# Kernel tuning notes

Hardware: AMD Instinct MI355X
Metric: run time of the kernel (lower is better)

## Reference

```python
import jax, jax.numpy as jnp
import numpy as np

D_MODEL = 192
D_INNER = 384   # expand=2
D_STATE = 16
D_CONV = 4
DT_RANK = 12    # ceil(192/16)
DEPTH = 4
STRIDE = 4
N_PATCH = 400   # 1600 // 4
NCLS = 1000
BATCH = 32
EPS = 1e-5


def setup_inputs() -> dict:
    key = jax.random.key(0)
    ks = iter(jax.random.split(key, 64))
    nrm = lambda shp, s=0.02: jax.random.normal(next(ks), shp, jnp.float32) * s
    inp = {}
    inp["imgs"] = jax.random.normal(next(ks), (BATCH, 1, 40, 40), jnp.float32)
    # StrideEmbed: conv1d(kernel=stride=4) == per-patch linear on [B,400,4]
    inp["patch_w"] = nrm((STRIDE, D_MODEL))
    inp["patch_b"] = jnp.zeros((D_MODEL,), jnp.float32)
    inp["cls_token"] = nrm((1, 1, D_MODEL))
    inp["pos_embed"] = nrm((1, N_PATCH + 1, D_MODEL))
    # per-block Mamba params, stacked on a leading depth axis
    inp["norm_ws"] = jnp.ones((DEPTH, D_MODEL), jnp.float32)
    inp["in_proj_ws"] = nrm((DEPTH, D_MODEL, 2 * D_INNER))
    inp["conv_ws"] = nrm((DEPTH, D_INNER, D_CONV), 0.2)
    inp["conv_bs"] = jnp.zeros((DEPTH, D_INNER), jnp.float32)
    inp["x_proj_ws"] = nrm((DEPTH, D_INNER, DT_RANK + 2 * D_STATE))
    inp["dt_proj_ws"] = nrm((DEPTH, DT_RANK, D_INNER), 0.1)
    # dt bias ~ inverse-softplus of small positive dt
    inp["dt_proj_bs"] = jnp.log(jnp.expm1(jnp.full((DEPTH, D_INNER), 0.01, jnp.float32)))
    inp["A_logs"] = jnp.log(jnp.broadcast_to(
        jnp.arange(1, D_STATE + 1, dtype=jnp.float32), (DEPTH, D_INNER, D_STATE)))
    inp["Ds"] = jnp.ones((DEPTH, D_INNER), jnp.float32)
    inp["out_proj_ws"] = nrm((DEPTH, D_INNER, D_MODEL))
    inp["norm_f_w"] = jnp.ones((D_MODEL,), jnp.float32)
    inp["head_w"] = nrm((D_MODEL, NCLS))
    inp["head_b"] = jnp.zeros((NCLS,), jnp.float32)
    return inp


def rmsnorm(x, w):
    return x * jax.lax.rsqrt(jnp.mean(x * x, axis=-1, keepdims=True) + EPS) * w


def mamba_mixer(x, in_w, conv_w, conv_b, xp_w, dt_w, dt_b, A_log, Dp, out_w):
    # x: [B, L, D_MODEL]
    B, L, _ = x.shape
    xz = x @ in_w                         # [B, L, 2*d_inner]
    u, z = jnp.split(xz, 2, axis=-1)
    # causal depthwise conv1d (kernel 4), truncated to L, then SiLU
    upad = jnp.pad(u, ((0, 0), (D_CONV - 1, 0), (0, 0)))
    uc = sum(upad[:, k:k + L, :] * conv_w[:, k] for k in range(D_CONV)) + conv_b
    uc = jax.nn.silu(uc)
    # input-dependent dt, B, C
    dbl = uc @ xp_w                       # [B, L, dt_rank + 2*d_state]
    dt = dbl[..., :DT_RANK]
    Bm = dbl[..., DT_RANK:DT_RANK + D_STATE]
    Cm = dbl[..., DT_RANK + D_STATE:]
    delta = jax.nn.softplus(dt @ dt_w + dt_b)           # [B, L, d_inner]
    A = -jnp.exp(A_log)                                  # [d_inner, d_state]
    dA = jnp.exp(delta[..., None] * A)                   # [B, L, d_inner, d_state]
    dBu = (delta * uc)[..., None] * Bm[:, :, None, :]    # [B, L, d_inner, d_state]

    def step(h, t):
        da, dbu, c = t
        h = da * h + dbu                                 # [B, d_inner, d_state]
        y = jnp.einsum('bds,bs->bd', h, c)
        return h, y

    h0 = jnp.zeros((B, D_INNER, D_STATE), x.dtype)
    _, ys = jax.lax.scan(step, h0, (jnp.moveaxis(dA, 1, 0),
                                    jnp.moveaxis(dBu, 1, 0),
                                    jnp.moveaxis(Cm, 1, 0)))
    y = jnp.moveaxis(ys, 0, 1) + uc * Dp                 # [B, L, d_inner]
    return (y * jax.nn.silu(z)) @ out_w


def reference(imgs, patch_w, patch_b, cls_token, pos_embed, norm_ws, in_proj_ws,
              conv_ws, conv_bs, x_proj_ws, dt_proj_ws, dt_proj_bs, A_logs, Ds,
              out_proj_ws, norm_f_w, head_w, head_b):
    B = imgs.shape[0]
    seq = imgs.reshape(B, N_PATCH, STRIDE)               # [B, 400, 4] (in_chans=1)
    x = seq @ patch_w + patch_b + pos_embed[:, :-1, :]   # patch embed + pos (cls pos is last)
    cls = cls_token + pos_embed[:, -1:, :]
    x = jnp.concatenate([x, jnp.broadcast_to(cls, (B, 1, D_MODEL))], axis=1)  # cls appended at end
    residual = None
    for i in range(DEPTH):
        residual = x if residual is None else x + residual  # fused add-norm, prenorm
        h = rmsnorm(residual, norm_ws[i])
        x = mamba_mixer(h, in_proj_ws[i], conv_ws[i], conv_bs[i], x_proj_ws[i],
                        dt_proj_ws[i], dt_proj_bs[i], A_logs[i], Ds[i], out_proj_ws[i])
    x = rmsnorm(x + residual, norm_f_w)                   # final fused add-norm, prenorm=False
    return x[:, -1, :] @ head_w + head_b                  # head on cls (last) token
```

## Files before the change

### kernel.cpp

```cpp
#include <hip/hip_runtime.h>
#include <hip/hip_bf16.h>
#include <hip/hip_fp16.h>

using bf16 = __hip_bfloat16;
typedef short short8 __attribute__((ext_vector_type(8)));
typedef float floatx4 __attribute__((ext_vector_type(4)));

#define LSEQ 401
#define NTOK 12832
#define NTOKP 12928
#define DM 192
#define DI 384
#define NB 32
#define NCH 13
#define CHT 32
#define LOG2E 1.4426950408889634f

#define O_IMGS   0
#define O_PW     51200
#define O_PB     51968
#define O_CLS    52160
#define O_POS    52352
#define O_NORMW  129344
#define O_INW    130112
#define O_CONVW  719936
#define O_CONVB  726080
#define O_XPW    727616
#define O_DTW    795200
#define O_DTB    813632
#define O_ALOG   815168
#define O_DS     839744
#define O_OUTW   841280
#define O_NORMF  1136192
#define O_HEADW  1136384
#define O_HEADB  1328384
#define WTOT     1329408

#define BO_INWT  0
#define BO_XPWT  589824
#define BO_OUTWT 688128
#define BFTOT_F  491520

__constant__ int g_sz[18] = {51200, 768, 192, 192, 76992, 768, 589824, 6144, 1536,
                             67584, 18432, 1536, 24576, 1536, 294912, 192, 192000, 1000};
__constant__ int g_off[18] = {O_IMGS, O_PW, O_PB, O_CLS, O_POS, O_NORMW, O_INW, O_CONVW,
                              O_CONVB, O_XPW, O_DTW, O_DTB, O_ALOG, O_DS, O_OUTW,
                              O_NORMF, O_HEADW, O_HEADB};

struct SrcPtrs { const void* p[18]; };

static __device__ __forceinline__ int probe_flag(const unsigned short* probe) {
    unsigned short u0 = probe[0];
    if (u0 == 0x3F80u) return 0;
    if (u0 == 0x3C00u) return 2;
    return 1;
}
static __device__ __forceinline__ float load_src(int flag, const void* p, long i) {
    if (flag == 0) return __bfloat162float(((const bf16*)p)[i]);
    if (flag == 2) return __half2float(((const __half*)p)[i]);
    return ((const float*)p)[i];
}
static __device__ __forceinline__ unsigned short f2b(float f) {
    bf16 h = __float2bfloat16(f);
    return *reinterpret_cast<unsigned short*>(&h);
}
static __device__ __forceinline__ float b2f_us(unsigned short us) {
    unsigned int ui = (unsigned int)us << 16;
    return __uint_as_float(ui);
}
static __device__ __forceinline__ float exp2fast(float x) {
    return __builtin_amdgcn_exp2f(x);
}

__global__ void convert_kernel(SrcPtrs sp, const unsigned short* __restrict__ probe,
                               float* __restrict__ dst) {
    int flag = probe_flag(probe);
    int which = blockIdx.y;
    int n = g_sz[which];
    const void* src = sp.p[which];
    float* d = dst + g_off[which];
    for (int i = blockIdx.x * blockDim.x + threadIdx.x; i < n; i += gridDim.x * blockDim.x)
        d[i] = load_src(flag, src, i);
}

__global__ void prep_wt_kernel(SrcPtrs sp, const unsigned short* __restrict__ probe,
                               unsigned short* __restrict__ bfw) {
    int flag = probe_flag(probe);
    int which = blockIdx.y, layer = blockIdx.z;
    int i = blockIdx.x * 256 + threadIdx.x;
    if (which == 0) {
        if (i >= 768 * 192) return;
        int n = i / 192, k = i % 192;
        float v = load_src(flag, sp.p[6], (long)layer * 147456 + (long)k * 768 + n);
        bfw[BO_INWT + (long)layer * 147456 + i] = f2b(v);
    } else if (which == 1) {
        if (i >= 64 * 384) return;
        int n = i / 384, k = i % 384;
        float v = (n < 44) ? load_src(flag, sp.p[9], (long)layer * 16896 + (long)k * 44 + n) : 0.f;
        bfw[BO_XPWT + (long)layer * 24576 + i] = f2b(v);
    } else {
        if (i >= 192 * 384) return;
        int n = i / 384, k = i % 384;
        float v = load_src(flag, sp.p[14], (long)layer * 73728 + (long)k * 192 + n);
        bfw[BO_OUTWT + (long)layer * 73728 + i] = f2b(v);
    }
}

__global__ __launch_bounds__(256) void resnorm_kernel(
    const float* __restrict__ x, float* __restrict__ res, unsigned short* __restrict__ hbf,
    const float* __restrict__ w, const float* __restrict__ W, int first) {
    int wv = threadIdx.x >> 6, lane = threadIdx.x & 63;
    long tok = (long)blockIdx.x * 4 + wv;
    long base = tok * DM + lane * 4;
    float4 v = make_float4(0.f, 0.f, 0.f, 0.f);
    bool real = (tok < NTOK);
    if (real && lane < 48) {
        if (first) {
            int b = (int)(tok / LSEQ), t = (int)(tok % LSEQ);
            int c = lane * 4;
            if (t < 400) {
                float s0 = W[O_IMGS + b * 1600 + t * 4 + 0];
                float s1 = W[O_IMGS + b * 1600 + t * 4 + 1];
                float s2 = W[O_IMGS + b * 1600 + t * 4 + 2];
                float s3 = W[O_IMGS + b * 1600 + t * 4 + 3];
                float4 p0 = *(const float4*)(W + O_PW + 0 * DM + c);
                float4 p1 = *(const float4*)(W + O_PW + 1 * DM + c);
                float4 p2 = *(const float4*)(W + O_PW + 2 * DM + c);
                float4 p3 = *(const float4*)(W + O_PW + 3 * DM + c);
                float4 pb = *(const float4*)(W + O_PB + c);
                float4 ps = *(const float4*)(W + O_POS + t * DM + c);
                v.x = s0 * p0.x + s1 * p1.x + s2 * p2.x + s3 * p3.x + pb.x + ps.x;
                v.y = s0 * p0.y + s1 * p1.y + s2 * p2.y + s3 * p3.y + pb.y + ps.y;
                v.z = s0 * p0.z + s1 * p1.z + s2 * p2.z + s3 * p3.z + pb.z + ps.z;
                v.w = s0 * p0.w + s1 * p1.w + s2 * p2.w + s3 * p3.w + pb.w + ps.w;
            } else {
                float4 cl = *(const float4*)(W + O_CLS + c);
                float4 ps = *(const float4*)(W + O_POS + 400 * DM + c);
                v.x = cl.x + ps.x; v.y = cl.y + ps.y;
                v.z = cl.z + ps.z; v.w = cl.w + ps.w;
            }
        } else {
            v = *(const float4*)(x + base);
            float4 r = *(const float4*)(res + base);
            v.x += r.x; v.y += r.y; v.z += r.z; v.w += r.w;
        }
        *(float4*)(res + base) = v;
    }
    float ss = v.x * v.x + v.y * v.y + v.z * v.z + v.w * v.w;
#pragma unroll
    for (int o = 1; o < 64; o <<= 1) ss += __shfl_xor(ss, o, 64);
    float inv = rsqrtf(ss * (1.f / DM) + 1e-5f);
    if (lane < 48) {
        if (real) {
            float4 w4 = *(const float4*)(w + lane * 4);
            ushort4 h;
            h.x = f2b(v.x * inv * w4.x); h.y = f2b(v.y * inv * w4.y);
            h.z = f2b(v.z * inv * w4.z); h.w = f2b(v.w * inv * w4.w);
            *(ushort4*)(hbf + base) = h;
        } else if (tok < NTOKP) {
            ushort4 h; h.x = h.y = h.z = h.w = 0;
            *(ushort4*)(hbf + base) = h;
        }
    }
}

template <int OUTBF>
__global__ __launch_bounds__(256) void gemm_mfma(
    const unsigned short* __restrict__ A, const unsigned short* __restrict__ Wt,
    void* __restrict__ C, int K, int N, int NC) {
    __shared__ unsigned short sA[64][72];
    __shared__ unsigned short sW[64][72];
    int tid = threadIdx.x;
    int w = tid >> 6, lane = tid & 63;
    int q = lane >> 4, m = lane & 15;
    long tok0 = (long)blockIdx.x * 64;
    int n0 = blockIdx.y * 64;
    floatx4 acc[4] = {};
    for (int k0 = 0; k0 < K; k0 += 64) {
        int slot = tid;
#pragma unroll
        for (int i = 0; i < 2; ++i, slot += 256) {
            int r = slot >> 3, c8 = (slot & 7) * 8;
            *(short8*)&sA[r][c8] = *(const short8*)(A + (tok0 + r) * K + k0 + c8);
            *(short8*)&sW[r][c8] = *(const short8*)(Wt + (long)(n0 + r) * K + k0 + c8);
        }
        __syncthreads();
#pragma unroll
        for (int q2 = 0; q2 < 64; q2 += 32) {
            short8 bfr = *(const short8*)&sA[w * 16 + m][q2 + q * 8];
#pragma unroll
            for (int nt = 0; nt < 4; ++nt) {
                short8 afr = *(const short8*)&sW[nt * 16 + m][q2 + q * 8];
                acc[nt] = __builtin_amdgcn_mfma_f32_16x16x32_bf16(afr, bfr, acc[nt], 0, 0, 0);
            }
        }
        __syncthreads();
    }
    long tok = tok0 + w * 16 + m;
#pragma unroll
    for (int nt = 0; nt < 4; ++nt) {
        int ch = n0 + nt * 16 + q * 4;
        if (OUTBF) {
            unsigned short* dst = (unsigned short*)C + tok * NC + ch;
            ushort4 h4;
            h4.x = f2b(acc[nt][0]); h4.y = f2b(acc[nt][1]);
            h4.z = f2b(acc[nt][2]); h4.w = f2b(acc[nt][3]);
            *(ushort4*)dst = h4;
        } else {
            float* dst = (float*)C + tok * NC + ch;
            if (ch + 3 < N) {
                *(float4*)dst = make_float4(acc[nt][0], acc[nt][1], acc[nt][2], acc[nt][3]);
            } else {
#pragma unroll
                for (int r = 0; r < 4; ++r)
                    if (ch + r < N) dst[r] = acc[nt][r];
            }
        }
    }
}

__global__ __launch_bounds__(256) void gemm_mfma128(
    const unsigned short* __restrict__ A, const unsigned short* __restrict__ Wt,
    unsigned short* __restrict__ C, int K, int NC) {
    __shared__ unsigned short sA[128][72];
    __shared__ unsigned short sW[64][72];
    int tid = threadIdx.x;
    int w = tid >> 6, lane = tid & 63;
    int q = lane >> 4, m = lane & 15;
    long tok0 = (long)blockIdx.x * 128;
    int n0 = blockIdx.y * 64;
    floatx4 acc[2][4] = {};
    for (int k0 = 0; k0 < K; k0 += 64) {
#pragma unroll
        for (int p = 0; p < 4; ++p) {
            int idx = tid + p * 256;
            int r = idx >> 3, c8 = (idx & 7) * 8;
            *(short8*)&sA[r][c8] = *(const short8*)(A + (tok0 + r) * K + k0 + c8);
        }
#pragma unroll
        for (int p = 0; p < 2; ++p) {
            int idx = tid + p * 256;
            int r = idx >> 3, c8 = (idx & 7) * 8;
            *(short8*)&sW[r][c8] = *(const short8*)(Wt + (long)(n0 + r) * K + k0 + c8);
        }
        __syncthreads();
#pragma unroll
        for (int q2 = 0; q2 < 64; q2 += 32) {
#pragma unroll
            for (int tf = 0; tf < 2; ++tf) {
                short8 bfr = *(const short8*)&sA[w * 32 + tf * 16 + m][q2 + q * 8];
#pragma unroll
                for (int nt = 0; nt < 4; ++nt) {
                    short8 afr = *(const short8*)&sW[nt * 16 + m][q2 + q * 8];
                    acc[tf][nt] = __builtin_amdgcn_mfma_f32_16x16x32_bf16(afr, bfr, acc[tf][nt], 0, 0, 0);
                }
            }
        }
        __syncthreads();
    }
#pragma unroll
    for (int tf = 0; tf < 2; ++tf) {
        long tok = tok0 + w * 32 + tf * 16 + m;
#pragma unroll
        for (int nt = 0; nt < 4; ++nt) {
            int ch = n0 + nt * 16 + q * 4;
            ushort4 h4;
            h4.x = f2b(acc[tf][nt][0]); h4.y = f2b(acc[tf][nt][1]);
            h4.z = f2b(acc[tf][nt][2]); h4.w = f2b(acc[tf][nt][3]);
            *(ushort4*)((unsigned short*)C + tok * NC + ch) = h4;
        }
    }
}

__global__ __launch_bounds__(256) void gemm_xproj_conv(
    const unsigned short* __restrict__ xzb, const unsigned short* __restrict__ Wt,
    const float* __restrict__ cw, const float* __restrict__ cb,
    unsigned short* __restrict__ ucb, float* __restrict__ dblP) {
    __shared__ unsigned short sA[64][72];
    __shared__ unsigned short sW[64][72];
    __shared__ float scw[128][4];
    __shared__ float scb[128];
    int tid = threadIdx.x;
    int w = tid >> 6, lane = tid & 63;
    int q = lane >> 4, m = lane & 15;
    long tok0 = (long)blockIdx.x * 64;
    int koff = blockIdx.y * 128;
    float* C = dblP + (long)blockIdx.y * NTOKP * 44;
    if (tid < 128) {
        scb[tid] = cb[koff + tid];
        *(float4*)&scw[tid][0] = *(const float4*)(cw + (koff + tid) * 4);
    }
    floatx4 acc[4] = {};
    for (int k0 = 0; k0 < 128; k0 += 64) {
        if (k0 == 0) __syncthreads();
        int slot = tid;
#pragma unroll
        for (int i = 0; i < 2; ++i, slot += 256) {
            int r = slot >> 3, c8 = (slot & 7) * 8;
            long tok = tok0 + r;
            int t = (int)(tok % LSEQ);
            int lk = k0 + c8;
            int kk = koff + lk;
            float res[8];
#pragma unroll
            for (int jj = 0; jj < 8; ++jj) res[jj] = scb[lk + jj];
#pragma unroll
            for (int j = 0; j < 4; ++j) {
                int off = 3 - j;
                if (t >= off) {
                    short8 v = *(const short8*)(xzb + (tok - off) * 768 + kk);
#pragma unroll
                    for (int jj = 0; jj < 8; ++jj)
                        res[jj] = fmaf(scw[lk + jj][j], b2f_us((unsigned short)v[jj]), res[jj]);
                }
            }
            short8 h8;
#pragma unroll
            for (int jj = 0; jj < 8; ++jj) {
                float sv = res[jj] / (1.f + __expf(-res[jj]));
                h8[jj] = (short)f2b(sv);
            }
            *(short8*)&sA[r][c8] = h8;
            *(short8*)(ucb + tok * DI + kk) = h8;
            *(short8*)&sW[r][c8] = *(const short8*)(Wt + (long)r * DI + koff + k0 + c8);
        }
        __syncthreads();
#pragma unroll
        for (int q2 = 0; q2 < 64; q2 += 32) {
            short8 bfr = *(const short8*)&sA[w * 16 + m][q2 + q * 8];
#pragma unroll
            for (int nt = 0; nt < 4; ++nt) {
                short8 afr = *(const short8*)&sW[nt * 16 + m][q2 + q * 8];
                acc[nt] = __builtin_amdgcn_mfma_f32_16x16x32_bf16(afr, bfr, acc[nt], 0, 0, 0);
            }
        }
        __syncthreads();
    }
    long tok = tok0 + w * 16 + m;
#pragma unroll
    for (int nt = 0; nt < 4; ++nt) {
        int ch = nt * 16 + q * 4;
        float* dst = C + tok * 44 + ch;
        if (ch + 3 < 44) {
            *(float4*)dst = make_float4(acc[nt][0], acc[nt][1], acc[nt][2], acc[nt][3]);
        } else {
#pragma unroll
            for (int r = 0; r < 4; ++r)
                if (ch + r < 44) dst[r] = acc[nt][r];
        }
    }
}

__global__ __launch_bounds__(256) void dbl_sum_kernel(const float* __restrict__ dblP,
                                                      float* __restrict__ dbl) {
    int i = blockIdx.x * 256 + threadIdx.x;
    if (i < NTOK * 44)
        dbl[i] = dblP[i] + dblP[(long)NTOKP * 44 + i] + dblP[(long)2 * NTOKP * 44 + i];
}

__global__ __launch_bounds__(256) void scan_sum_kernel(
    const float* __restrict__ dbl, const unsigned short* __restrict__ ucb,
    const float* __restrict__ dtw, const float* __restrict__ dtb,
    const float* __restrict__ Alog, unsigned short* __restrict__ deltaBuf,
    float* __restrict__ Aprod, float* __restrict__ Hend) {
    int ch = blockIdx.x, b = blockIdx.y;
    int tid = threadIdx.x;
    int shalf = tid & 1;
    int d = blockIdx.z * 128 + (tid >> 1);
    int t0 = ch * CHT;
    long tokb = (long)b * LSEQ + t0;
    int tmax = min(CHT, LSEQ - t0);
    bool last = (ch == NCH - 1);
    __shared__ float sdt[CHT][12];
    __shared__ float sB[CHT][16];
    for (int i = tid; i < tmax * 12; i += 256) {
        int r = i / 12, k = i % 12;
        sdt[r][k] = dbl[(tokb + r) * 44 + k];
    }
    if (!last) {
        for (int i = tid; i < CHT * 16; i += 256) {
            int r = i >> 4, s = i & 15;
            sB[r][s] = dbl[(tokb + r) * 44 + 12 + s];
        }
    }
    float dtwr[12];
#pragma unroll
    for (int k = 0; k < 12; ++k) dtwr[k] = dtw[k * DI + d];
    float bias = dtb[d];
    float a[8];
#pragma unroll
    for (int s = 0; s < 8; ++s) a[s] = -__expf(Alog[d * 16 + shalf * 8 + s]) * LOG2E;
    float h[8] = {};
    float sumd = 0.f;
    __syncthreads();
    float u0 = b2f_us(ucb[tokb * DI + d]);
    float u1 = b2f_us(ucb[(tokb + min(1, tmax - 1)) * DI + d]);
#pragma unroll 2
    for (int t = 0; t < tmax; ++t) {
        int tp = min(t + 2, tmax - 1);
        float u2 = b2f_us(ucb[(tokb + tp) * DI + d]);
        float acc = bias;
#pragma unroll
        for (int k = 0; k < 12; ++k) acc = fmaf(sdt[t][k], dtwr[k], acc);
        float delta = (acc > 20.f) ? acc : __logf(1.f + __expf(acc));
        delta = b2f_us(f2b(delta));
        if (shalf == 0) deltaBuf[(tokb + t) * DI + d] = f2b(delta);
        if (!last) {
            float du = delta * u0;
            sumd += delta;
            float Bv[8];
            *(float4*)&Bv[0] = *(const float4*)&sB[t][shalf * 8];
            *(float4*)&Bv[4] = *(const float4*)&sB[t][shalf * 8 + 4];
#pragma unroll
            for (int s = 0; s < 8; ++s) {
                float da = exp2fast(delta * a[s]);
                h[s] = fmaf(da, h[s], du * Bv[s]);
            }
        }
        u0 = u1; u1 = u2;
    }
    if (!last) {
        long idx = (((long)b * NCH + ch) * DI + d) * 16 + shalf * 8;
        float ap[8], he[8];
#pragma unroll
        for (int s = 0; s < 8; ++s) { ap[s] = exp2fast(a[s] * sumd); he[s] = h[s]; }
        *(float4*)(Aprod + idx) = *(float4*)&ap[0];
        *(float4*)(Aprod + idx + 4) = *(float4*)&ap[4];
        *(float4*)(Hend + idx) = *(float4*)&he[0];
        *(float4*)(Hend + idx + 4) = *(float4*)&he[4];
    }
}

__global__ __launch_bounds__(256) void scan_combine_kernel(
    const float* __restrict__ Ap, const float* __restrict__ He, float* __restrict__ hinit) {
    long gid = (long)blockIdx.x * 256 + threadIdx.x;
    int b = (int)(gid / 6144);
    int r = (int)(gid % 6144);
    float carry = 0.f;
#pragma unroll
    for (int j = 0; j < NCH; ++j) {
        long idx = ((long)b * NCH + j) * 6144 + r;
        hinit[idx] = carry;
        if (j < NCH - 1) carry = fmaf(Ap[idx], carry, He[idx]);
    }
}

__global__ __launch_bounds__(256) void scan_main_kernel(
    const unsigned short* __restrict__ deltaBuf, const unsigned short* __restrict__ ucb,
    const unsigned short* __restrict__ xzb, const float* __restrict__ Alog,
    const float* __restrict__ Dvec, const float* __restrict__ hinit,
    const float* __restrict__ dbl, unsigned short* __restrict__ ybf) {
    int ch = blockIdx.x, b = blockIdx.y;
    int tid = threadIdx.x;
    int shalf = tid & 1;
    int d = blockIdx.z * 128 + (tid >> 1);
    int t0 = ch * CHT;
    long tokb = (long)b * LSEQ + t0;
    int tmax = min(CHT, LSEQ - t0);
    __shared__ float sB[CHT][16], sC[CHT][16];
    for (int i = tid; i < CHT * 16; i += 256) {
        int r = i >> 4, s = i & 15;
        bool ok = (r < tmax);
        sB[r][s] = ok ? dbl[(tokb + r) * 44 + 12 + s] : 0.f;
        sC[r][s] = ok ? dbl[(tokb + r) * 44 + 28 + s] : 0.f;
    }
    float a[8];
#pragma unroll
    for (int s = 0; s < 8; ++s) a[s] = -__expf(Alog[d * 16 + shalf * 8 + s]) * LOG2E;
    float h[8];
    long hidx = (((long)b * NCH + ch) * DI + d) * 16 + shalf * 8;
    *(float4*)&h[0] = *(const float4*)(hinit + hidx);
    *(float4*)&h[4] = *(const float4*)(hinit + hidx + 4);
    float Dp = Dvec[d];
    __syncthreads();
    int t1i = min(1, tmax - 1);
    float d0 = b2f_us(deltaBuf[tokb * DI + d]);
    float u0 = b2f_us(ucb[tokb * DI + d]);
    float z0 = b2f_us(xzb[tokb * 768 + DI + d]);
    float d1 = b2f_us(deltaBuf[(tokb + t1i) * DI + d]);
    float u1 = b2f_us(ucb[(tokb + t1i) * DI + d]);
    float z1 = b2f_us(xzb[(tokb + t1i) * 768 + DI + d]);
#pragma unroll 2
    for (int t = 0; t < tmax; ++t) {
        int tp = min(t + 2, tmax - 1);
        float d2 = b2f_us(deltaBuf[(tokb + tp) * DI + d]);
        float u2 = b2f_us(ucb[(tokb + tp) * DI + d]);
        float z2 = b2f_us(xzb[(tokb + tp) * 768 + DI + d]);
        float Bv[8], Cv[8];
        *(float4*)&Bv[0] = *(const float4*)&sB[t][shalf * 8];
        *(float4*)&Bv[4] = *(const float4*)&sB[t][shalf * 8 + 4];
        *(float4*)&Cv[0] = *(const float4*)&sC[t][shalf * 8];
        *(float4*)&Cv[4] = *(const float4*)&sC[t][shalf * 8 + 4];
        float du = d0 * u0;
        float y0 = 0.f, y1 = 0.f, y2 = 0.f, y3 = 0.f;
#pragma unroll
        for (int s = 0; s < 8; s += 4) {
            float da0 = exp2fast(d0 * a[s]);
            float da1 = exp2fast(d0 * a[s + 1]);
            float da2 = exp2fast(d0 * a[s + 2]);
            float da3 = exp2fast(d0 * a[s + 3]);
            h[s]     = fmaf(da0, h[s],     du * Bv[s]);
            h[s + 1] = fmaf(da1, h[s + 1], du * Bv[s + 1]);
            h[s + 2] = fmaf(da2, h[s + 2], du * Bv[s + 2]);
            h[s + 3] = fmaf(da3, h[s + 3], du * Bv[s + 3]);
            y0 = fmaf(h[s],     Cv[s],     y0);
            y1 = fmaf(h[s + 1], Cv[s + 1], y1);
            y2 = fmaf(h[s + 2], Cv[s + 2], y2);
            y3 = fmaf(h[s + 3], Cv[s + 3], y3);
        }
        float p = (y0 + y1) + (y2 + y3);
        p += __shfl_xor(p, 1, 64);
        if (shalf == 0) {
            float y = fmaf(u0, Dp, p);
            float gz = z0 / (1.f + __expf(-z0));
            ybf[(tokb + t) * DI + d] = f2b(y * gz);
        }
        d0 = d1; u0 = u1; z0 = z1;
        d1 = d2; u1 = u2; z1 = z2;
    }
}

__global__ __launch_bounds__(128) void head_kernel(
    const float* __restrict__ x, const float* __restrict__ res,
    const float* __restrict__ nf, const float* __restrict__ hw,
    const float* __restrict__ hb, const unsigned short* __restrict__ probe,
    void* __restrict__ out) {
    int b = blockIdx.y;
    int n = blockIdx.x * 128 + threadIdx.x;
    long tok = (long)b * LSEQ + 400;
    __shared__ float vs[DM];
    __shared__ float red[2];
    float ss = 0.f;
    for (int i = threadIdx.x; i < DM; i += 128) {
        float v = x[tok * DM + i] + res[tok * DM + i];
        vs[i] = v;
        ss = fmaf(v, v, ss);
    }
#pragma unroll
    for (int o = 1; o < 64; o <<= 1) ss += __shfl_xor(ss, o, 64);
    if ((threadIdx.x & 63) == 0) red[threadIdx.x >> 6] = ss;
    __syncthreads();
    float inv = rsqrtf((red[0] + red[1]) * (1.f / DM) + 1e-5f);
    for (int i = threadIdx.x; i < DM; i += 128) vs[i] = vs[i] * inv * nf[i];
    __syncthreads();
    if (n < 1000) {
        float acc = hb[n];
#pragma unroll 4
        for (int c = 0; c < DM; ++c) acc = fmaf(vs[c], hw[c * 1000 + n], acc);
        int flag = probe_flag(probe);
        if (flag == 0)      ((bf16*)out)[b * 1000 + n] = (bf16)acc;
        else if (flag == 2) ((__half*)out)[b * 1000 + n] = __float2half(acc);
        else                ((float*)out)[b * 1000 + n] = acc;
    }
}

extern "C" void kernel_launch(void* const* d_in, const int* in_sizes, int n_in,
                              void* d_out, int out_size, void* d_ws, size_t ws_size,
                              hipStream_t stream) {
    float* ws = (float*)d_ws;
    float* Wr = ws;
    unsigned short* bfw = (unsigned short*)(ws + WTOT);
    float* act   = ws + WTOT + BFTOT_F;
    float* resT  = act;
    float* xB    = resT + (long)NTOKP * DM;
    float* dbl   = xB + (long)NTOKP * DM;
    float* dblP  = dbl + (long)NTOKP * 44;
    float* Aprod = dblP + (long)3 * NTOKP * 44;
    float* Hend  = Aprod + (long)NB * NCH * 6144;
    float* hinit = Hend + (long)NB * NCH * 6144;
    unsigned short* deltaB = (unsigned short*)(hinit + (long)NB * NCH * 6144);
    unsigned short* hbf = deltaB + (long)NTOKP * DI;
    unsigned short* xzb = hbf + (long)NTOKP * DM;
    unsigned short* ucb = xzb + (long)NTOKP * 768;
    unsigned short* ybf = ucb + (long)NTOKP * DI;

    const unsigned short* probe = (const unsigned short*)d_in[5];

    SrcPtrs sp;
    for (int i = 0; i < 18; ++i) sp.p[i] = d_in[i];
    convert_kernel<<<dim3(64, 18), 256, 0, stream>>>(sp, probe, Wr);
    prep_wt_kernel<<<dim3(576, 3, 4), 256, 0, stream>>>(sp, probe, bfw);

    for (int i = 0; i < 4; ++i) {
        resnorm_kernel<<<NTOKP / 4, 256, 0, stream>>>(
            xB, resT, hbf, Wr + O_NORMW + i * DM, Wr, i == 0);
        gemm_mfma128<<<dim3(101, 12), 256, 0, stream>>>(
            hbf, bfw + BO_INWT + (long)i * 147456, xzb, 192, 768);
        gemm_xproj_conv<<<dim3(202, 3), 256, 0, stream>>>(
            xzb, bfw + BO_XPWT + (long)i * 24576,
            Wr + O_CONVW + i * 1536, Wr + O_CONVB + i * DI, ucb, dblP);
        dbl_sum_kernel<<<(NTOK * 44 + 255) / 256, 256, 0, stream>>>(dblP, dbl);
        scan_sum_kernel<<<dim3(NCH, NB, 3), 256, 0, stream>>>(
            dbl, ucb, Wr + O_DTW + i * 4608, Wr + O_DTB + i * DI,
            Wr + O_ALOG + i * 6144, deltaB, Aprod, Hend);
        scan_combine_kernel<<<(NB * 6144) / 256, 256, 0, stream>>>(Aprod, Hend, hinit);
        scan_main_kernel<<<dim3(NCH, NB, 3), 256, 0, stream>>>(
            deltaB, ucb, xzb, Wr + O_ALOG + i * 6144, Wr + O_DS + i * DI,
            hinit, dbl, ybf);
        gemm_mfma<0><<<dim3(202, 3), 256, 0, stream>>>(
            ybf, bfw + BO_OUTWT + (long)i * 73728, xB, 384, 192, 192);
    }

    head_kernel<<<dim3(8, NB), 128, 0, stream>>>(
        xB, resT, Wr + O_NORMF, Wr + O_HEADW, Wr + O_HEADB, probe, d_out);
}
```

Measured before the change: 603.7 us.

## Fuse split-K partial reduction into scan_sum and halve scan chunk length

Removes the separate dbl_sum kernel. scan_sum now sums the three split-K partial x_proj slabs directly into shared memory, and the z==0 blocks write the reduced dbl back for later kernels. It also halves the chunk length (CHT 32→16, NCH 13→26), doubling the number of scan blocks so the sequential chunked scan has more parallelism. The cost is more chunk states for scan_combine to process and redundant partial-sum reads across the three z-blocks. It also assumes scan_combine and scan_main use NCH/CHT consistently.

```diff
diff --git a/kernel.cpp b/kernel.cpp
--- a/kernel.cpp
+++ b/kernel.cpp
@@ -12,8 +12,9 @@
 #define DM 192
 #define DI 384
 #define NB 32
-#define NCH 13
-#define CHT 32
+#define NCH 26
+#define CHT 16
+#define SLAB ((long)NTOKP * 44)
 #define LOG2E 1.4426950408889634f
 
 #define O_IMGS   0
@@ -351,18 +352,11 @@
     }
 }
 
-__global__ __launch_bounds__(256) void dbl_sum_kernel(const float* __restrict__ dblP,
-                                                      float* __restrict__ dbl) {
-    int i = blockIdx.x * 256 + threadIdx.x;
-    if (i < NTOK * 44)
-        dbl[i] = dblP[i] + dblP[(long)NTOKP * 44 + i] + dblP[(long)2 * NTOKP * 44 + i];
-}
-
 __global__ __launch_bounds__(256) void scan_sum_kernel(
-    const float* __restrict__ dbl, const unsigned short* __restrict__ ucb,
+    const float* __restrict__ dblP, const unsigned short* __restrict__ ucb,
     const float* __restrict__ dtw, const float* __restrict__ dtb,
     const float* __restrict__ Alog, unsigned short* __restrict__ deltaBuf,
-    float* __restrict__ Aprod, float* __restrict__ Hend) {
+    float* __restrict__ Aprod, float* __restrict__ Hend, float* __restrict__ dbl) {
     int ch = blockIdx.x, b = blockIdx.y;
     int tid = threadIdx.x;
     int shalf = tid & 1;
@@ -371,17 +365,11 @@
     long tokb = (long)b * LSEQ + t0;
     int tmax = min(CHT, LSEQ - t0);
     bool last = (ch == NCH - 1);
-    __shared__ float sdt[CHT][12];
-    __shared__ float sB[CHT][16];
-    for (int i = tid; i < tmax * 12; i += 256) {
-        int r = i / 12, k = i % 12;
-        sdt[r][k] = dbl[(tokb + r) * 44 + k];
-    }
-    if (!last) {
-        for (int i = tid; i < CHT * 16; i += 256) {
-            int r = i >> 4, s = i & 15;
-            sB[r][s] = dbl[(tokb + r) * 44 + 12 + s];
-        }
+    __shared__ float sdbl[CHT][44];
+    for (int i = tid; i < tmax * 44; i += 256) {
+        int r = i / 44, k = i % 44;
+        long o = (tokb + r) * 44 + k;
+        sdbl[r][k] = dblP[o] + dblP[o + SLAB] + dblP[o + 2 * SLAB];
     }
     float dtwr[12];
 #pragma unroll
@@ -393,6 +381,12 @@
     float h[8] = {};
     float sumd = 0.f;
     __syncthreads();
+    if (blockIdx.z == 0) {
+        for (int i = tid; i < tmax * 44; i += 256) {
+            int r = i / 44, k = i % 44;
+            dbl[(tokb + r) * 44 + k] = sdbl[r][k];
+        }
+    }
     float u0 = b2f_us(ucb[tokb * DI + d]);
     float u1 = b2f_us(ucb[(tokb + min(1, tmax - 1)) * DI + d]);
 #pragma unroll 2
@@ -401,7 +395,7 @@
         float u2 = b2f_us(ucb[(tokb + tp) * DI + d]);
         float acc = bias;
 #pragma unroll
-        for (int k = 0; k < 12; ++k) acc = fmaf(sdt[t][k], dtwr[k], acc);
+        for (int k = 0; k < 12; ++k) acc = fmaf(sdbl[t][k], dtwr[k], acc);
         float delta = (acc > 20.f) ? acc : __logf(1.f + __expf(acc));
         delta = b2f_us(f2b(delta));
         if (shalf == 0) deltaBuf[(tokb + t) * DI + d] = f2b(delta);
@@ -409,8 +403,8 @@
             float du = delta * u0;
             sumd += delta;
             float Bv[8];
-            *(float4*)&Bv[0] = *(const float4*)&sB[t][shalf * 8];
-            *(float4*)&Bv[4] = *(const float4*)&sB[t][shalf * 8 + 4];
+            *(float4*)&Bv[0] = *(const float4*)&sdbl[t][12 + shalf * 8];
+            *(float4*)&Bv[4] = *(const float4*)&sdbl[t][12 + shalf * 8 + 4];
 #pragma unroll
             for (int s = 0; s < 8; ++s) {
                 float da = exp2fast(delta * a[s]);
@@ -565,7 +559,7 @@
     float* xB    = resT + (long)NTOKP * DM;
     float* dbl   = xB + (long)NTOKP * DM;
     float* dblP  = dbl + (long)NTOKP * 44;
-    float* Aprod = dblP + (long)3 * NTOKP * 44;
+    float* Aprod = dblP + 3 * SLAB;
     float* Hend  = Aprod + (long)NB * NCH * 6144;
     float* hinit = Hend + (long)NB * NCH * 6144;
     unsigned short* deltaB = (unsigned short*)(hinit + (long)NB * NCH * 6144);
@@ -589,10 +583,9 @@
         gemm_xproj_conv<<<dim3(202, 3), 256, 0, stream>>>(
             xzb, bfw + BO_XPWT + (long)i * 24576,
             Wr + O_CONVW + i * 1536, Wr + O_CONVB + i * DI, ucb, dblP);
-        dbl_sum_kernel<<<(NTOK * 44 + 255) / 256, 256, 0, stream>>>(dblP, dbl);
         scan_sum_kernel<<<dim3(NCH, NB, 3), 256, 0, stream>>>(
-            dbl, ucb, Wr + O_DTW + i * 4608, Wr + O_DTB + i * DI,
-            Wr + O_ALOG + i * 6144, deltaB, Aprod, Hend);
+            dblP, ucb, Wr + O_DTW + i * 4608, Wr + O_DTB + i * DI,
+            Wr + O_ALOG + i * 6144, deltaB, Aprod, Hend, dbl);
         scan_combine_kernel<<<(NB * 6144) / 256, 256, 0, stream>>>(Aprod, Hend, hinit);
         scan_main_kernel<<<dim3(NCH, NB, 3), 256, 0, stream>>>(
             deltaB, ucb, xzb, Wr + O_ALOG + i * 6144, Wr + O_DS + i * DI,
```

Result: no change. 599.3 us (-0.7%).
